# Optimization experiments

Measured on AMD Instinct MI355X. Metric: run time of the kernel, lower is better.

## Reference

```python
import jax, jax.numpy as jnp
import numpy as np
from jax import lax

WIN_SIZE = 11
SIGMA = 1.5
WEIGHTS = jnp.array([0.0448, 0.2856, 0.3001, 0.2363, 0.1333], dtype=jnp.float32)
C1 = (0.01 * 1.0) ** 2  # val_range = 1.0
C2 = (0.03 * 1.0) ** 2


def gaussian_kernel2d(kernel_size, sigma):
    g = jnp.arange(kernel_size, dtype=jnp.float32) - kernel_size // 2
    g = jnp.exp(-(g ** 2) / (2.0 * sigma ** 2))
    g = g / g.sum()
    return jnp.outer(g, g)  # [k, k]


def depthwise_conv(x, k2d):
    # x: [B, C, H, W]; same gaussian window applied per-channel (groups=C), VALID padding
    C = x.shape[1]
    w = jnp.broadcast_to(k2d, (C, 1) + k2d.shape).astype(x.dtype)
    return lax.conv_general_dilated(x, w, (1, 1), 'VALID',
                                    feature_group_count=C,
                                    dimension_numbers=('NCHW', 'OIHW', 'NCHW'))


def ssim_index(x, y, k2d, nonnegative=True):
    # returns (ss, cs) each of shape [B, C] (spatial mean, per channel)
    m1 = depthwise_conv(x, k2d)
    m2 = depthwise_conv(y, k2d)
    m12 = m1 * m2
    m1s = m1 * m1
    m2s = m2 * m2
    v1 = depthwise_conv(x * x, k2d) - m1s
    v2 = depthwise_conv(y * y, k2d) - m2s
    cov = depthwise_conv(x * y, k2d) - m12
    cs = (2.0 * cov + C2) / (v1 + v2 + C2)
    ss = (2.0 * m12 + C1) / (m1s + m2s + C1) * cs
    ss = ss.reshape(ss.shape[0], ss.shape[1], -1).mean(axis=-1)
    cs = cs.reshape(cs.shape[0], cs.shape[1], -1).mean(axis=-1)
    if nonnegative:
        ss = jnp.maximum(ss, 0.0)
        cs = jnp.maximum(cs, 0.0)
    return ss, cs


def avg_pool2(x):
    # F.avg_pool2d(kernel_size=2). Input spatial dims are even at every scale
    # (512 -> 32), so ceil_mode never pads; plain 2x2/2 mean pooling is exact.
    s = lax.reduce_window(x, jnp.array(0.0, x.dtype), lax.add,
                          (1, 1, 2, 2), (1, 1, 2, 2), 'VALID')
    return s * 0.25


def setup_inputs() -> dict:
    key = jax.random.key(0)
    k1, k2 = jax.random.split(key)
    B, C, H, W = 4, 12, 512, 512
    pred = jax.random.normal(k1, (B, C, H, W), dtype=jnp.float32)
    target = jax.random.randint(k2, (B, H, W), 0, C, dtype=jnp.int64)
    return {"pred": pred, "target": target}


def reference(pred, target):
    # MS_SSIMLoss.forward with process_input=True, nonnegative=True.
    # The per-class python loop in the original is an independent depthwise
    # computation per channel -> vectorized here as a C-channel grouped conv;
    # loss = mean over classes of (1 - mean over batch of msss) == 1 - mean(msss).
    num_classes = pred.shape[1]
    x = jax.nn.softmax(pred, axis=1)
    y = jax.nn.one_hot(target, num_classes, dtype=pred.dtype).transpose(0, 3, 1, 2)
    k2d = gaussian_kernel2d(WIN_SIZE, SIGMA)
    m = WEIGHTS.shape[0]
    vals = []
    for i in range(m):
        if i > 0:
            x = avg_pool2(x)
            y = avg_pool2(y)
        ss, cs = ssim_index(x, y, k2d, nonnegative=True)
        vals.append(cs if i + 1 < m else ss)
    stacked = jnp.stack(vals, axis=-1)  # [B, C, m]
    msss = jnp.prod(stacked ** WEIGHTS, axis=-1)  # [B, C]
    return 1.0 - msss.mean()
```

## Files before the change

### kernel.cpp

```cpp
#include <hip/hip_runtime.h>

#define NCH 12
#define NB  4
#define BC  48
#define HW0 (512 * 512)

#define GK_INIT { 0.00102840f, 0.00759863f, 0.03600078f, 0.10936081f, \
                  0.21300541f, 0.26601164f, 0.21300541f, 0.10936081f, \
                  0.03600078f, 0.00759863f, 0.00102840f }

__global__ void k_denom(const float4* __restrict__ pred, float4* __restrict__ U,
                        double* __restrict__ acc) {
    if (blockIdx.x == 0) {
        for (int t = threadIdx.x; t < 480; t += 256) acc[t] = 0.0;
    }
    int i = blockIdx.x * blockDim.x + threadIdx.x;
    if (i >= NB * (HW0 / 4)) return;
    int b = i >> 16;
    int p = i & 65535;
    const float4* base = pred + (((size_t)b * NCH) << 16) + p;
    float4 s = make_float4(0.f, 0.f, 0.f, 0.f);
#pragma unroll
    for (int c = 0; c < NCH; ++c) {
        float4 v = base[(size_t)c << 16];
        s.x += expf(v.x); s.y += expf(v.y);
        s.z += expf(v.z); s.w += expf(v.w);
    }
    float4 u;
    u.x = 1.f / s.x; u.y = 1.f / s.y; u.z = 1.f / s.z; u.w = 1.f / s.w;
    U[((size_t)b << 16) + p] = u;
}

__global__ __launch_bounds__(256, 5)
void k_ssim0(const float* __restrict__ pred, const float* __restrict__ U,
             const int* __restrict__ tgt, double* __restrict__ acc,
             float* __restrict__ Xp, unsigned short* __restrict__ Yp) {
    constexpr int SS = 43;
    constexpr int TS = 34;
    constexpr int H = 512, W = 512, OH = 502, OW = 502, tilesX = 16;
    __shared__ float sx[42 * SS + 4];
    __shared__ float4 tm4[42 * TS];
    __shared__ unsigned long long ybits[30];
    __shared__ float red[8];

    const float gk[11] = GK_INIT;

    const int bc = blockIdx.y;
    const int tile = blockIdx.x;
    const int ty = tile / tilesX, tx = tile - ty * tilesX;
    const int oy = ty * 32, ox = tx * 32;
    const int tid = threadIdx.x;
    const bool interior = (oy + 41 < H) && (ox + 41 < W);

    const int b = bc / NCH, cls = bc - (bc / NCH) * NCH;
    const float* Pb = pred + (((size_t)b * NCH + cls) << 18);
    const float* Ub = U + ((size_t)b << 18);
    const int* Tb = tgt + ((size_t)b << 18);

    {
        int r = tid / 42, c = tid - (tid / 42) * 42;
#pragma unroll
        for (int k = 0; k < 7; ++k) {
            bool inr = (k < 6) || (tid < 228);
            int gy = oy + r, gx = ox + c;
            bool ld = inr && (interior || (gy < H && gx < W));
            float xv = 0.f;
            bool bit = false;
            if (ld) {
                int off = gy * W + gx;
                xv = expf(Pb[off]) * Ub[off];
                bit = (Tb[off] == cls);
            }
            unsigned long long mk = __ballot(bit);
            if ((tid & 63) == 0) ybits[(tid >> 6) + (k << 2)] = mk;
            if (inr) sx[r * SS + c] = xv;
            c += 4; r += 6;
            if (c >= 42) { c -= 42; r += 1; }
        }
        if (tid == 0) { ybits[28] = 0ull; ybits[29] = 0ull; }
    }
    __syncthreads();

    if (tid < 252) {
        int rr = tid / 6, s = tid - (tid / 6) * 6;
        int c0 = s * 6;
        const float* px = sx + rr * SS + c0;
        float ac0[6] = {}, ac1[6] = {}, ac2[6] = {}, ac3[6] = {};
        unsigned long long win;
        {
            int i0 = rr * 42 + c0;
            int w = i0 >> 6, sh = i0 & 63;
            unsigned long long lo = ybits[w], hi = ybits[w + 1];
            win = sh ? ((lo >> sh) | (hi << (64 - sh))) : lo;
        }
#pragma unroll
        for (int j = 0; j < 16; ++j) {
            float xv = px[j];
            float xx = xv * xv;
            bool bit = (win >> j) & 1;
            float yv = bit ? 1.f : 0.f;
            float xy = bit ? xv : 0.f;
#pragma unroll
            for (int o = 0; o < 6; ++o) {
                int kk = j - o;
                if (kk >= 0 && kk <= 10) {
                    float g = gk[kk];
                    ac0[o] = fmaf(g, xv, ac0[o]);
                    ac1[o] = fmaf(g, yv, ac1[o]);
                    ac2[o] = fmaf(g, xx, ac2[o]);
                    ac3[o] = fmaf(g, xy, ac3[o]);
                }
            }
        }
        int ob = rr * TS + c0;
#pragma unroll
        for (int o = 0; o < 6; ++o)
            if (c0 + o < 32)
                tm4[ob + o] = make_float4(ac0[o], ac1[o], ac2[o], ac3[o]);
    }
    __syncthreads();

    const float C1 = 1e-4f, C2 = 9e-4f;
    const int cc = tid & 31, rg = tid >> 5, r0 = rg << 2;
    float a0[4] = {}, a1[4] = {}, a2[4] = {}, a3[4] = {};
    const int vb = r0 * TS + cc;
#pragma unroll
    for (int k = 0; k < 14; ++k) {
        float4 tv = tm4[vb + k * TS];
#pragma unroll
        for (int j = 0; j < 4; ++j) {
            int kk = k - j;
            if (kk >= 0 && kk <= 10) {
                float g = gk[kk];
                a0[j] = fmaf(g, tv.x, a0[j]);
                a1[j] = fmaf(g, tv.y, a1[j]);
                a2[j] = fmaf(g, tv.z, a2[j]);
                a3[j] = fmaf(g, tv.w, a3[j]);
            }
        }
    }
    float cs_l = 0.f, ss_l = 0.f;
    const bool colok = (ox + cc < OW);
#pragma unroll
    for (int j = 0; j < 4; ++j) {
        if (colok && (oy + r0 + j < OH)) {
            float m1 = a0[j], m2 = a1[j];
            float sxx = a2[j], sxy_ = a3[j];
            float m11 = m1 * m1, m22 = m2 * m2, m12 = m1 * m2;
            float v1 = sxx - m11, v2 = m2 - m22, cov = sxy_ - m12;
            float d1 = m11 + m22 + C1, d2 = v1 + v2 + C2;
            float n2 = 2.f * cov + C2;
            float q = 1.f / (d1 * d2);
            cs_l = fmaf(n2 * d1, q, cs_l);
            ss_l = fmaf((2.f * m12 + C1) * n2, q, ss_l);
        }
    }

    {
        int py = tid >> 4, pxx = tid & 15;
        int s0 = (py * 2) * SS + pxx * 2;
        float xs = 0.25f * (sx[s0] + sx[s0 + 1] + sx[s0 + SS] + sx[s0 + SS + 1]);
        size_t oidx = ((size_t)bc * 256 + (oy >> 1) + py) * 256 + (ox >> 1) + pxx;
        Xp[oidx] = xs;
        int i0 = (py * 2) * 42 + pxx * 2, i1 = i0 + 42;
        unsigned c0 = (unsigned)((ybits[i0 >> 6] >> (i0 & 63)) & 1ull);
        unsigned c1 = (unsigned)((ybits[(i0 + 1) >> 6] >> ((i0 + 1) & 63)) & 1ull);
        unsigned c2 = (unsigned)((ybits[i1 >> 6] >> (i1 & 63)) & 1ull);
        unsigned c3 = (unsigned)((ybits[(i1 + 1) >> 6] >> ((i1 + 1) & 63)) & 1ull);
        Yp[oidx] = (unsigned short)((c0 + c1 + c2 + c3) << 6);
    }

    for (int off = 32; off; off >>= 1) {
        cs_l += __shfl_down(cs_l, off);
        ss_l += __shfl_down(ss_l, off);
    }
    int wv = tid >> 6, ln = tid & 63;
    if (ln == 0) { red[wv] = cs_l; red[4 + wv] = ss_l; }
    __syncthreads();
    if (tid == 0) {
        double cs_b = (double)red[0] + (double)red[1] + (double)red[2] + (double)red[3];
        double ss_b = (double)red[4] + (double)red[5] + (double)red[6] + (double)red[7];
        atomicAdd(&acc[bc], cs_b);
        atomicAdd(&acc[48 + bc], ss_b);
    }
}

template <int PIN>
__device__ __forceinline__ void ssim_tile_g(
    const float* __restrict__ Xs, const unsigned short* __restrict__ Ys,
    int H, int W, int OH, int OW, int tilesX, int tile, int bc,
    double* __restrict__ acc, int scale,
    float* __restrict__ Xp, unsigned short* __restrict__ Yp, bool pool,
    float* sx, float4* tm4, float* tm5, unsigned short* syu, float* red) {
    constexpr int SS = 43;
    constexpr int TS = 34;
    const float gk[11] = GK_INIT;

    const int ty = tile / tilesX, tx = tile - ty * tilesX;
    const int oy = ty * 32, ox = tx * 32;
    const int tid = threadIdx.x;
    const bool interior = (oy + 41 < H) && (ox + 41 < W);

    const int SC = (PIN == 0) ? 1 : (PIN == 1 ? 2 : 4);
    const int SW = W * SC;
    const float* Xb = Xs + (size_t)bc * H * W * SC * SC;
    const unsigned short* Yb = Ys + (size_t)bc * H * W * SC * SC;

    {
        int r = tid / 42, c = tid - (tid / 42) * 42;
#pragma unroll
        for (int k = 0; k < 7; ++k) {
            bool inr = (k < 6) || (tid < 228);
            int gy = oy + r, gx = ox + c;
            bool ld = inr && (interior || (gy < H && gx < W));
            float xv = 0.f;
            unsigned short yv = 0;
            if (ld) {
                if constexpr (PIN == 0) {
                    int off = gy * SW + gx;
                    xv = Xb[off];
                    yv = Yb[off];
                } else if constexpr (PIN == 1) {
                    const float* q = Xb + (2 * gy) * SW + 2 * gx;
                    xv = 0.25f * (q[0] + q[1] + q[SW] + q[SW + 1]);
                    const unsigned short* qy = Yb + (2 * gy) * SW + 2 * gx;
                    yv = (unsigned short)(((unsigned)qy[0] + qy[1] + qy[SW] + qy[SW + 1]) >> 2);
                } else {
                    const float* q = Xb + (4 * gy) * SW + 4 * gx;
                    const unsigned short* qy = Yb + (4 * gy) * SW + 4 * gx;
                    float s = 0.f; unsigned us = 0;
#pragma unroll
                    for (int a = 0; a < 4; ++a) {
#pragma unroll
                        for (int e = 0; e < 4; ++e) {
                            s += q[a * SW + e];
                            us += qy[a * SW + e];
                        }
                    }
                    xv = s * (1.f / 16.f);
                    yv = (unsigned short)(us >> 4);
                }
            }
            if (inr) { sx[r * SS + c] = xv; syu[r * SS + c] = yv; }
            c += 4; r += 6;
            if (c >= 42) { c -= 42; r += 1; }
        }
    }
    __syncthreads();

    if (tid < 252) {
        int rr = tid / 6, s = tid - (tid / 6) * 6;
        int c0 = s * 6;
        const float* px = sx + rr * SS + c0;
        const unsigned short* pyu = syu + rr * SS + c0;
        float ac0[6] = {}, ac1[6] = {}, ac2[6] = {}, ac3[6] = {}, ac4[6] = {};
#pragma unroll
        for (int j = 0; j < 16; ++j) {
            float xv = px[j];
            float xx = xv * xv;
            float yv = (float)pyu[j];
            float xy = xv * yv;
            float yy = yv * yv;
#pragma unroll
            for (int o = 0; o < 6; ++o) {
                int kk = j - o;
                if (kk >= 0 && kk <= 10) {
                    float g = gk[kk];
                    ac0[o] = fmaf(g, xv, ac0[o]);
                    ac1[o] = fmaf(g, yv, ac1[o]);
                    ac2[o] = fmaf(g, xx, ac2[o]);
                    ac3[o] = fmaf(g, xy, ac3[o]);
                    ac4[o] = fmaf(g, yy, ac4[o]);
                }
            }
        }
        int ob = rr * TS + c0;
#pragma unroll
        for (int o = 0; o < 6; ++o) {
            if (c0 + o < 32) {
                tm4[ob + o] = make_float4(ac0[o], ac1[o], ac2[o], ac3[o]);
                tm5[ob + o] = ac4[o];
            }
        }
    }
    __syncthreads();

    const float C1 = 1e-4f, C2 = 9e-4f;
    const int cc = tid & 31, rg = tid >> 5, r0 = rg << 2;
    float a0[4] = {}, a1[4] = {}, a2[4] = {}, a3[4] = {}, a4[4] = {};
    const int vb = r0 * TS + cc;
#pragma unroll
    for (int k = 0; k < 14; ++k) {
        float4 tv = tm4[vb + k * TS];
        float t4 = tm5[vb + k * TS];
#pragma unroll
        for (int j = 0; j < 4; ++j) {
            int kk = k - j;
            if (kk >= 0 && kk <= 10) {
                float g = gk[kk];
                a0[j] = fmaf(g, tv.x, a0[j]);
                a1[j] = fmaf(g, tv.y, a1[j]);
                a2[j] = fmaf(g, tv.z, a2[j]);
                a3[j] = fmaf(g, tv.w, a3[j]);
                a4[j] = fmaf(g, t4, a4[j]);
            }
        }
    }
    float cs_l = 0.f, ss_l = 0.f;
    const bool colok = (ox + cc < OW);
#pragma unroll
    for (int j = 0; j < 4; ++j) {
        if (colok && (oy + r0 + j < OH)) {
            float m1 = a0[j];
            float m2 = a1[j] * (1.f / 256.f);
            float sxx = a2[j];
            float sxy_ = a3[j] * (1.f / 256.f);
            float syy_ = a4[j] * (1.f / 65536.f);
            float m11 = m1 * m1, m22 = m2 * m2, m12 = m1 * m2;
            float v1 = sxx - m11, v2 = syy_ - m22, cov = sxy_ - m12;
            float d1 = m11 + m22 + C1, d2 = v1 + v2 + C2;
            float n2 = 2.f * cov + C2;
            float q = 1.f / (d1 * d2);
            cs_l = fmaf(n2 * d1, q, cs_l);
            ss_l = fmaf((2.f * m12 + C1) * n2, q, ss_l);
        }
    }

    if (pool) {
        int py = tid >> 4, pxx = tid & 15;
        int s0 = (py * 2) * SS + pxx * 2;
        float xs = 0.25f * (sx[s0] + sx[s0 + 1] + sx[s0 + SS] + sx[s0 + SS + 1]);
        int PH = H >> 1, PW = W >> 1;
        size_t oidx = ((size_t)bc * PH + (oy >> 1) + py) * PW + (ox >> 1) + pxx;
        Xp[oidx] = xs;
        unsigned sum = (unsigned)syu[s0] + syu[s0 + 1] + syu[s0 + SS] + syu[s0 + SS + 1];
        Yp[oidx] = (unsigned short)(sum >> 2);
    }

    for (int offs = 32; offs; offs >>= 1) {
        cs_l += __shfl_down(cs_l, offs);
        ss_l += __shfl_down(ss_l, offs);
    }
    int wv = tid >> 6, ln = tid & 63;
    if (ln == 0) { red[wv] = cs_l; red[4 + wv] = ss_l; }
    __syncthreads();
    if (tid == 0) {
        double cs_b = (double)red[0] + (double)red[1] + (double)red[2] + (double)red[3];
        double ss_b = (double)red[4] + (double)red[5] + (double)red[6] + (double)red[7];
        atomicAdd(&acc[scale * 96 + bc], cs_b);
        atomicAdd(&acc[scale * 96 + 48 + bc], ss_b);
    }
}

#define GENERIC_LDS \
    __shared__ float sx[42 * 43 + 4]; \
    __shared__ float4 tm4[42 * 34]; \
    __shared__ float tm5[42 * 34]; \
    __shared__ unsigned short syu[42 * 43 + 4]; \
    __shared__ float red[8];

__global__ __launch_bounds__(256, 4)
void k_ssim1(const float* __restrict__ X1, const unsigned short* __restrict__ Y1,
             double* __restrict__ acc, float* __restrict__ X2,
             unsigned short* __restrict__ Y2) {
    GENERIC_LDS
    ssim_tile_g<0>(X1, Y1, 256, 256, 246, 246, 8, blockIdx.x, blockIdx.y,
                   acc, 1, X2, Y2, true, sx, tm4, tm5, syu, red);
}

__global__ __launch_bounds__(256, 4)
void k_s234(const float* __restrict__ X2, const unsigned short* __restrict__ Y2,
            double* __restrict__ acc) {
    GENERIC_LDS
    const int gb = blockIdx.x;

    if (gb < 768) {
        ssim_tile_g<0>(X2, Y2, 128, 128, 118, 118, 4, gb & 15, gb >> 4,
                       acc, 2, nullptr, nullptr, false, sx, tm4, tm5, syu, red);
    } else if (gb < 960) {
        int t = gb - 768;
        ssim_tile_g<1>(X2, Y2, 64, 64, 54, 54, 2, t & 3, t >> 2,
                       acc, 3, nullptr, nullptr, false, sx, tm4, tm5, syu, red);
    } else {
        ssim_tile_g<2>(X2, Y2, 32, 32, 22, 22, 1, 0, gb - 960,
                       acc, 4, nullptr, nullptr, false, sx, tm4, tm5, syu, red);
    }
}

__global__ void k_final(const double* __restrict__ acc, float* __restrict__ out) {
    const float wts[5] = {0.0448f, 0.2856f, 0.3001f, 0.2363f, 0.1333f};
    const float cnt[5] = {252004.f, 60516.f, 13924.f, 2916.f, 484.f};
    int tid = threadIdx.x;
    float msss = 0.f;
    if (tid < BC) {
        msss = 1.f;
#pragma unroll
        for (int s = 0; s < 5; ++s) {
            double a = (s < 4) ? acc[s * 96 + tid] : acc[s * 96 + 48 + tid];
            float v = fmaxf((float)(a / (double)cnt[s]), 0.f);
            msss *= powf(v, wts[s]);
        }
    }
    for (int off = 32; off; off >>= 1) msss += __shfl_down(msss, off);
    if (tid == 0) out[0] = 1.f - msss * (1.f / (float)BC);
}

extern "C" void kernel_launch(void* const* d_in, const int* in_sizes, int n_in,
                              void* d_out, int out_size, void* d_ws, size_t ws_size,
                              hipStream_t stream) {
    const float* pred = (const float*)d_in[0];
    const int*   tgt  = (const int*)d_in[1];
    float* out = (float*)d_out;

    double* acc = (double*)d_ws;
    float* U  = (float*)(acc + 480);
    float* X1 = U + (size_t)NB * 512 * 512;
    float* X2 = X1 + (size_t)BC * 256 * 256;
    unsigned short* Y1 = (unsigned short*)(X2 + (size_t)BC * 128 * 128);
    unsigned short* Y2 = Y1 + (size_t)BC * 256 * 256;

    k_denom<<<(NB * (HW0 / 4) + 255) / 256, 256, 0, stream>>>(
        (const float4*)pred, (float4*)U, acc);

    k_ssim0<<<dim3(256, BC), 256, 0, stream>>>(pred, U, tgt, acc, X1, Y1);

    k_ssim1<<<dim3(64, BC), 256, 0, stream>>>(X1, Y1, acc, X2, Y2);

    k_s234<<<dim3(1008), 256, 0, stream>>>(X2, Y2, acc);

    k_final<<<1, 64, 0, stream>>>(acc, out);
}
```

Before: 252.7 us.

## Merge scales 1-4 into one kernel reading pooled scale-1 data directly

Replaces the separate scale-1 kernel (which also wrote pooled X2/Y2) and the scales 2-4 kernel with a single launch. Every remaining scale now reads from X1/Y1 and pools on the fly with factor 2^PIN, which removes a launch, a dependency barrier and the X2/Y2 round trip through memory. The cost is more redundant global reads at the coarser scales (up to 8x8 per pixel at scale 4) and a divergent mix of tile types inside one grid. The shared tile stride also changes from 34 to 35, likely to reduce LDS bank conflicts.

```diff
diff --git a/kernel.cpp b/kernel.cpp
--- a/kernel.cpp
+++ b/kernel.cpp
@@ -36,7 +36,7 @@
              const int* __restrict__ tgt, double* __restrict__ acc,
              float* __restrict__ Xp, unsigned short* __restrict__ Yp) {
     constexpr int SS = 43;
-    constexpr int TS = 34;
+    constexpr int TS = 35;
     constexpr int H = 512, W = 512, OH = 502, OW = 502, tilesX = 16;
     __shared__ float sx[42 * SS + 4];
     __shared__ float4 tm4[42 * TS];
@@ -190,10 +190,9 @@
     const float* __restrict__ Xs, const unsigned short* __restrict__ Ys,
     int H, int W, int OH, int OW, int tilesX, int tile, int bc,
     double* __restrict__ acc, int scale,
-    float* __restrict__ Xp, unsigned short* __restrict__ Yp, bool pool,
     float* sx, float4* tm4, float* tm5, unsigned short* syu, float* red) {
     constexpr int SS = 43;
-    constexpr int TS = 34;
+    constexpr int TS = 35;
     const float gk[11] = GK_INIT;
 
     const int ty = tile / tilesX, tx = tile - ty * tilesX;
@@ -201,7 +200,7 @@
     const int tid = threadIdx.x;
     const bool interior = (oy + 41 < H) && (ox + 41 < W);
 
-    const int SC = (PIN == 0) ? 1 : (PIN == 1 ? 2 : 4);
+    constexpr int SC = 1 << PIN;
     const int SW = W * SC;
     const float* Xb = Xs + (size_t)bc * H * W * SC * SC;
     const unsigned short* Yb = Ys + (size_t)bc * H * W * SC * SC;
@@ -220,25 +219,20 @@
                     int off = gy * SW + gx;
                     xv = Xb[off];
                     yv = Yb[off];
-                } else if constexpr (PIN == 1) {
-                    const float* q = Xb + (2 * gy) * SW + 2 * gx;
-                    xv = 0.25f * (q[0] + q[1] + q[SW] + q[SW + 1]);
-                    const unsigned short* qy = Yb + (2 * gy) * SW + 2 * gx;
-                    yv = (unsigned short)(((unsigned)qy[0] + qy[1] + qy[SW] + qy[SW + 1]) >> 2);
                 } else {
-                    const float* q = Xb + (4 * gy) * SW + 4 * gx;
-                    const unsigned short* qy = Yb + (4 * gy) * SW + 4 * gx;
+                    const float* q = Xb + (SC * gy) * SW + SC * gx;
+                    const unsigned short* qy = Yb + (SC * gy) * SW + SC * gx;
                     float s = 0.f; unsigned us = 0;
 #pragma unroll
-                    for (int a = 0; a < 4; ++a) {
-#pragma unroll
-                        for (int e = 0; e < 4; ++e) {
+                    for (int a = 0; a < SC; ++a) {
+#pragma unroll
+                        for (int e = 0; e < SC; ++e) {
                             s += q[a * SW + e];
                             us += qy[a * SW + e];
                         }
                     }
-                    xv = s * (1.f / 16.f);
-                    yv = (unsigned short)(us >> 4);
+                    xv = s * (1.f / (float)(SC * SC));
+                    yv = (unsigned short)(us >> (2 * PIN));
                 }
             }
             if (inr) { sx[r * SS + c] = xv; syu[r * SS + c] = yv; }
@@ -326,17 +320,6 @@
         }
     }
 
-    if (pool) {
-        int py = tid >> 4, pxx = tid & 15;
-        int s0 = (py * 2) * SS + pxx * 2;
-        float xs = 0.25f * (sx[s0] + sx[s0 + 1] + sx[s0 + SS] + sx[s0 + SS + 1]);
-        int PH = H >> 1, PW = W >> 1;
-        size_t oidx = ((size_t)bc * PH + (oy >> 1) + py) * PW + (ox >> 1) + pxx;
-        Xp[oidx] = xs;
-        unsigned sum = (unsigned)syu[s0] + syu[s0 + 1] + syu[s0 + SS] + syu[s0 + SS + 1];
-        Yp[oidx] = (unsigned short)(sum >> 2);
-    }
-
     for (int offs = 32; offs; offs >>= 1) {
         cs_l += __shfl_down(cs_l, offs);
         ss_l += __shfl_down(ss_l, offs);
@@ -352,38 +335,30 @@
     }
 }
 
-#define GENERIC_LDS \
-    __shared__ float sx[42 * 43 + 4]; \
-    __shared__ float4 tm4[42 * 34]; \
-    __shared__ float tm5[42 * 34]; \
-    __shared__ unsigned short syu[42 * 43 + 4]; \
+__global__ __launch_bounds__(256, 4)
+void k_rest(const float* __restrict__ X1, const unsigned short* __restrict__ Y1,
+            double* __restrict__ acc) {
+    __shared__ float sx[42 * 43 + 4];
+    __shared__ float4 tm4[42 * 35];
+    __shared__ float tm5[42 * 35];
+    __shared__ unsigned short syu[42 * 43 + 4];
     __shared__ float red[8];
-
-__global__ __launch_bounds__(256, 4)
-void k_ssim1(const float* __restrict__ X1, const unsigned short* __restrict__ Y1,
-             double* __restrict__ acc, float* __restrict__ X2,
-             unsigned short* __restrict__ Y2) {
-    GENERIC_LDS
-    ssim_tile_g<0>(X1, Y1, 256, 256, 246, 246, 8, blockIdx.x, blockIdx.y,
-                   acc, 1, X2, Y2, true, sx, tm4, tm5, syu, red);
-}
-
-__global__ __launch_bounds__(256, 4)
-void k_s234(const float* __restrict__ X2, const unsigned short* __restrict__ Y2,
-            double* __restrict__ acc) {
-    GENERIC_LDS
     const int gb = blockIdx.x;
 
-    if (gb < 768) {
-        ssim_tile_g<0>(X2, Y2, 128, 128, 118, 118, 4, gb & 15, gb >> 4,
-                       acc, 2, nullptr, nullptr, false, sx, tm4, tm5, syu, red);
-    } else if (gb < 960) {
-        int t = gb - 768;
-        ssim_tile_g<1>(X2, Y2, 64, 64, 54, 54, 2, t & 3, t >> 2,
-                       acc, 3, nullptr, nullptr, false, sx, tm4, tm5, syu, red);
+    if (gb < 3072) {
+        ssim_tile_g<0>(X1, Y1, 256, 256, 246, 246, 8, gb & 63, gb >> 6,
+                       acc, 1, sx, tm4, tm5, syu, red);
+    } else if (gb < 3840) {
+        int t = gb - 3072;
+        ssim_tile_g<1>(X1, Y1, 128, 128, 118, 118, 4, t & 15, t >> 4,
+                       acc, 2, sx, tm4, tm5, syu, red);
+    } else if (gb < 4032) {
+        int t = gb - 3840;
+        ssim_tile_g<2>(X1, Y1, 64, 64, 54, 54, 2, t & 3, t >> 2,
+                       acc, 3, sx, tm4, tm5, syu, red);
     } else {
-        ssim_tile_g<2>(X2, Y2, 32, 32, 22, 22, 1, 0, gb - 960,
-                       acc, 4, nullptr, nullptr, false, sx, tm4, tm5, syu, red);
+        ssim_tile_g<3>(X1, Y1, 32, 32, 22, 22, 1, 0, gb - 4032,
+                       acc, 4, sx, tm4, tm5, syu, red);
     }
 }
 
@@ -415,18 +390,14 @@
     double* acc = (double*)d_ws;
     float* U  = (float*)(acc + 480);
     float* X1 = U + (size_t)NB * 512 * 512;
-    float* X2 = X1 + (size_t)BC * 256 * 256;
-    unsigned short* Y1 = (unsigned short*)(X2 + (size_t)BC * 128 * 128);
-    unsigned short* Y2 = Y1 + (size_t)BC * 256 * 256;
+    unsigned short* Y1 = (unsigned short*)(X1 + (size_t)BC * 256 * 256);
 
     k_denom<<<(NB * (HW0 / 4) + 255) / 256, 256, 0, stream>>>(
         (const float4*)pred, (float4*)U, acc);
 
     k_ssim0<<<dim3(256, BC), 256, 0, stream>>>(pred, U, tgt, acc, X1, Y1);
 
-    k_ssim1<<<dim3(64, BC), 256, 0, stream>>>(X1, Y1, acc, X2, Y2);
-
-    k_s234<<<dim3(1008), 256, 0, stream>>>(X2, Y2, acc);
+    k_rest<<<dim3(4080), 256, 0, stream>>>(X1, Y1, acc);
 
     k_final<<<1, 64, 0, stream>>>(acc, out);
 }
```

After: 253.4 us. About the same (+0.3%).
